# Kernel optimization log

Hardware: AMD Instinct MI355X
Metric: run time of the kernel (lower is better)

## Reference

```python
import jax, jax.numpy as jnp
import numpy as np

B, T, N, A_DIM = 64, 512, 256, 8
TAU, DT, J1 = 10.0, 1.0, 0.1
BUMP_WIDTH_FACTOR = 10.0


def setup_inputs() -> dict:
    key = jax.random.key(0)
    k1, k2, k3 = jax.random.split(key, 3)
    action_signal = jax.random.normal(k1, (B, T, A_DIM), dtype=jnp.float32)
    # learned params, init as in torch: randn / sqrt(N)
    Wo = jax.random.normal(k2, (N, N), dtype=jnp.float32) / np.sqrt(N).astype(np.float32)
    Wa = jax.random.normal(k3, (A_DIM, N, N), dtype=jnp.float32) / np.sqrt(N).astype(np.float32)
    # buffers
    idx = jnp.arange(N, dtype=jnp.float32)
    angle_diff = 2.0 * jnp.pi * (idx[:, None] - idx[None, :]) / N
    W_delta7 = jnp.cos(angle_diff)                       # [N, N]
    J0 = -0.1 * jnp.ones((N, N), dtype=jnp.float32)      # baseline connectivity
    # initial bump at angle pi (create_initial_bump with default r_init=None)
    centers = (jnp.full((B,), jnp.pi, dtype=jnp.float32) * N / (2.0 * jnp.pi))[:, None]
    d = jnp.abs(idx[None, :] - centers)
    dist = jnp.minimum(d, N - d)
    width = N / BUMP_WIDTH_FACTOR
    bump = jnp.exp(-(dist ** 2) / (2.0 * width ** 2))
    r_init = bump / jnp.linalg.norm(bump, axis=1, keepdims=True)  # [B, N]
    return {"action_signal": action_signal, "r_init": r_init, "Wo": Wo,
            "Wa": Wa, "J0": J0, "W_delta7": W_delta7}


def reference(action_signal, r_init, Wo, Wa, J0, W_delta7):
    # W_eff[b] = J0 + J1*Wo + sum_a A[b,t,a] * Wa[a]; never materialize [B,T,N,N]
    W_base = J0 + J1 * Wo                         # [N, N], action-independent part
    leak = jnp.float32(DT / TAU)

    def step(r, A_t):                             # r: [B,N], A_t: [B,A]
        Wr = jnp.einsum('aij,bj->abi', Wa, r)     # [A, B, N] per-action matvec
        rec = r @ W_base.T + jnp.einsum('ba,abi->bi', A_t, Wr)  # [B, N]
        r_new = r + leak * (-r + jnp.tanh(rec))   # leaky-rate update
        d7 = r_new @ W_delta7.T                   # output projection [B, N]
        bump = d7 / jnp.linalg.norm(d7, axis=1, keepdims=True)  # normalized r_delta7
        return r_new, (r_new, bump)

    _, (r_hist, bump_hist) = jax.lax.scan(step, r_init,
                                          jnp.swapaxes(action_signal, 0, 1))
    # scan stacks over time -> [T, B, N]; return [B, T, N]
    return jnp.swapaxes(r_hist, 0, 1), jnp.swapaxes(bump_hist, 0, 1)
```

## Files before the change

### kernel.cpp

```cpp
#include <hip/hip_runtime.h>
#include <math.h>


#define BATCH 64
#define TT    512
#define NN    256
#define ADIM  8
#define NMAT  9
#define ROWS  (NMAT * NN)
#define GROUPS (ROWS / 64)
#define NTHR  576
#define KC    32

__global__ __launch_bounds__(256)
void build_wt_kernel(const float* __restrict__ Wo,
                     const float* __restrict__ Wa,
                     const float* __restrict__ J0,
                     uint4* __restrict__ Wt)
{
  const int q    = blockIdx.x * 256 + threadIdx.x;
  const int lane = q & 63;
  const int kc   = (q >> 6) & 31;
  const int g    = q >> 11;
  const int row  = g * 64 + lane;
  const int mat  = row >> 8;
  const int i    = row & 255;
  const int c0   = kc * 8;
  float v[8];
  if (mat == 0) {
    #pragma unroll
    for (int j = 0; j < 8; ++j)
      v[j] = J0[i * NN + c0 + j] + 0.1f * Wo[i * NN + c0 + j];
  } else {
    const float* src = Wa + ((size_t)(mat - 1) * NN + i) * NN + c0;
    #pragma unroll
    for (int j = 0; j < 8; ++j) v[j] = src[j];
  }
  uint p[4];
  #pragma unroll
  for (int j = 0; j < 4; ++j) {
    _Float16 hl = (_Float16)v[2 * j];
    _Float16 hh = (_Float16)v[2 * j + 1];
    unsigned short sl, sh;
    __builtin_memcpy(&sl, &hl, 2);
    __builtin_memcpy(&sh, &hh, 2);
    p[j] = (uint)sl | ((uint)sh << 16);
  }
  Wt[(size_t)(g * KC + kc) * 64 + lane] = make_uint4(p[0], p[1], p[2], p[3]);
}

__device__ __forceinline__ float f16lo(uint u) {
  unsigned short s = (unsigned short)(u & 0xFFFFu);
  _Float16 h; __builtin_memcpy(&h, &s, 2);
  return (float)h;
}
__device__ __forceinline__ float f16hi(uint u) {
  unsigned short s = (unsigned short)(u >> 16);
  _Float16 h; __builtin_memcpy(&h, &s, 2);
  return (float)h;
}

__device__ __forceinline__ float dot8(uint4 w, float4 ra, float4 rb) {
  float s;
  s  = f16lo(w.x) * ra.x;
  s += f16hi(w.x) * ra.y;
  s += f16lo(w.y) * ra.z;
  s += f16hi(w.y) * ra.w;
  s += f16lo(w.z) * rb.x;
  s += f16hi(w.z) * rb.y;
  s += f16lo(w.w) * rb.z;
  s += f16hi(w.w) * rb.w;
  return s;
}

__global__ __launch_bounds__(NTHR, 1)
void ring_main_kernel(const float* __restrict__ act,
                      const float* __restrict__ r_init,
                      const float* __restrict__ Wd7,
                      const uint4* __restrict__ Wt,
                      float* __restrict__ out)
{
  __shared__ float r_s[NN];
  __shared__ float m_s[ROWS];
  __shared__ float cvec[NN], svec[NN];
  __shared__ float at_s[ADIM];
  __shared__ float cs_s[4][2];
  __shared__ float sums_s[3];

  const int tid  = threadIdx.x;
  const int wv   = tid >> 6;
  const int lane = tid & 63;
  const int b    = blockIdx.x;

  float* out_r = out;
  float* out_b = out + (size_t)BATCH * TT * NN;

  for (int idx = tid; idx < NN; idx += NTHR) {
    cvec[idx] = Wd7[idx * NN];
    svec[idx] = Wd7[idx * NN + 64];
    r_s[idx]  = r_init[b * NN + idx];
  }
  __syncthreads();
  if (tid == 0) {
    float a = 0.f, c2 = 0.f, c = 0.f;
    for (int j = 0; j < NN; ++j) {
      const float cj = cvec[j], sj = svec[j];
      a += cj * cj; c2 += cj * sj; c += sj * sj;
    }
    sums_s[0] = a; sums_s[1] = c2; sums_s[2] = c;
  }
  __syncthreads();

  const int g0 = wv * 4;
  const uint4* base0 = Wt + (size_t)(g0 + 0) * KC * 64 + lane;
  const uint4* base1 = Wt + (size_t)(g0 + 1) * KC * 64 + lane;
  const uint4* base2 = Wt + (size_t)(g0 + 2) * KC * 64 + lane;
  const uint4* base3 = Wt + (size_t)(g0 + 3) * KC * 64 + lane;

  for (int t = 0; t < TT; ++t) {
    if (tid < ADIM) at_s[tid] = act[((size_t)b * TT + t) * ADIM + tid];

    float a0 = 0.f, a1 = 0.f, a2 = 0.f, a3 = 0.f;
    uint4 w0 = base0[0], w1 = base1[0], w2 = base2[0], w3 = base3[0];
    #pragma unroll 4
    for (int k = 0; k < KC; ++k) {
      const float4 ra = *(const float4*)&r_s[k * 8];
      const float4 rb = *(const float4*)&r_s[k * 8 + 4];
      const int kn = (k + 1) & (KC - 1);
      uint4 n0 = base0[kn * 64], n1 = base1[kn * 64];
      uint4 n2 = base2[kn * 64], n3 = base3[kn * 64];
      a0 += dot8(w0, ra, rb);
      a1 += dot8(w1, ra, rb);
      a2 += dot8(w2, ra, rb);
      a3 += dot8(w3, ra, rb);
      w0 = n0; w1 = n1; w2 = n2; w3 = n3;
    }
    m_s[(g0 + 0) * 64 + lane] = a0;
    m_s[(g0 + 1) * 64 + lane] = a1;
    m_s[(g0 + 2) * 64 + lane] = a2;
    m_s[(g0 + 3) * 64 + lane] = a3;
    __syncthreads();

    if (tid < NN) {
      const int i = tid;
      float rec = m_s[i];
      #pragma unroll
      for (int a = 0; a < ADIM; ++a) rec += at_s[a] * m_s[(1 + a) * NN + i];
      const float ro = r_s[i];
      const float rn = ro + 0.1f * (tanhf(rec) - ro);
      r_s[i] = rn;
      out_r[((size_t)b * TT + t) * NN + i] = rn;
      float cp = cvec[i] * rn, sp = svec[i] * rn;
      #pragma unroll
      for (int m = 1; m < 64; m <<= 1) {
        cp += __shfl_xor(cp, m);
        sp += __shfl_xor(sp, m);
      }
      if (lane == 0) { cs_s[wv][0] = cp; cs_s[wv][1] = sp; }
    }
    __syncthreads();

    if (tid < NN) {
      const int i = tid;
      const float C = cs_s[0][0] + cs_s[1][0] + cs_s[2][0] + cs_s[3][0];
      const float S = cs_s[0][1] + cs_s[1][1] + cs_s[2][1] + cs_s[3][1];
      const float n2 = sums_s[0] * C * C + 2.f * sums_s[1] * C * S
                     + sums_s[2] * S * S;
      out_b[((size_t)b * TT + t) * NN + i] =
          (cvec[i] * C + svec[i] * S) * (1.0f / sqrtf(n2));
    }
  }
}

extern "C" void kernel_launch(void* const* d_in, const int* in_sizes, int n_in,
                              void* d_out, int out_size, void* d_ws, size_t ws_size,
                              hipStream_t stream) {
  const float* act    = (const float*)d_in[0];
  const float* r_init = (const float*)d_in[1];
  const float* Wo     = (const float*)d_in[2];
  const float* Wa     = (const float*)d_in[3];
  const float* J0     = (const float*)d_in[4];
  const float* Wd7    = (const float*)d_in[5];
  float* out = (float*)d_out;
  uint4* Wt  = (uint4*)d_ws;

  hipLaunchKernelGGL(build_wt_kernel, dim3(288), dim3(256), 0, stream,
                     Wo, Wa, J0, Wt);
  hipLaunchKernelGGL(ring_main_kernel, dim3(BATCH), dim3(NTHR), 0, stream,
                     act, r_init, Wd7, (const uint4*)Wt, out);
}
```

Baseline: 6.234 ms.

## Keep per-thread weight slices in registers and use fdot2 with split-f16 state

```diff
diff --git a/kernel.cpp b/kernel.cpp
--- a/kernel.cpp
+++ b/kernel.cpp
@@ -8,9 +8,27 @@
 #define ADIM  8
 #define NMAT  9
 #define ROWS  (NMAT * NN)
-#define GROUPS (ROWS / 64)
-#define NTHR  576
-#define KC    32
+#define NTHR  768
+#define KQ    32
+#define REG_KQ2 16
+
+typedef _Float16 half2_t __attribute__((ext_vector_type(2)));
+
+static __device__ __forceinline__ half2_t u2h(unsigned int u) {
+  union { unsigned int u; half2_t h; } c; c.u = u; return c.h;
+}
+
+static __device__ __forceinline__ void dot4(uint4 w, uint4 rh, uint4 rl,
+                                            float& ah, float& al) {
+  ah = __builtin_amdgcn_fdot2(u2h(w.x), u2h(rh.x), ah, false);
+  ah = __builtin_amdgcn_fdot2(u2h(w.y), u2h(rh.y), ah, false);
+  ah = __builtin_amdgcn_fdot2(u2h(w.z), u2h(rh.z), ah, false);
+  ah = __builtin_amdgcn_fdot2(u2h(w.w), u2h(rh.w), ah, false);
+  al = __builtin_amdgcn_fdot2(u2h(w.x), u2h(rl.x), al, false);
+  al = __builtin_amdgcn_fdot2(u2h(w.y), u2h(rl.y), al, false);
+  al = __builtin_amdgcn_fdot2(u2h(w.z), u2h(rl.z), al, false);
+  al = __builtin_amdgcn_fdot2(u2h(w.w), u2h(rl.w), al, false);
+}
 
 __global__ __launch_bounds__(256)
 void build_wt_kernel(const float* __restrict__ Wo,
@@ -18,14 +36,15 @@
                      const float* __restrict__ J0,
                      uint4* __restrict__ Wt)
 {
-  const int q    = blockIdx.x * 256 + threadIdx.x;
-  const int lane = q & 63;
-  const int kc   = (q >> 6) & 31;
-  const int g    = q >> 11;
-  const int row  = g * 64 + lane;
-  const int mat  = row >> 8;
-  const int i    = row & 255;
-  const int c0   = kc * 8;
+  const int q     = blockIdx.x * 256 + threadIdx.x;
+  const int gkq   = q / NTHR;
+  const int tid_t = q - gkq * NTHR;
+  const int g     = gkq >> 5;
+  const int kq    = gkq & 31;
+  const int row   = g * NTHR + tid_t;
+  const int mat   = row >> 8;
+  const int i     = row & 255;
+  const int c0    = kq * 8;
   float v[8];
   if (mat == 0) {
     #pragma unroll
@@ -36,7 +55,7 @@
     #pragma unroll
     for (int j = 0; j < 8; ++j) v[j] = src[j];
   }
-  uint p[4];
+  unsigned int p[4];
   #pragma unroll
   for (int j = 0; j < 4; ++j) {
     _Float16 hl = (_Float16)v[2 * j];
@@ -44,33 +63,9 @@
     unsigned short sl, sh;
     __builtin_memcpy(&sl, &hl, 2);
     __builtin_memcpy(&sh, &hh, 2);
-    p[j] = (uint)sl | ((uint)sh << 16);
-  }
-  Wt[(size_t)(g * KC + kc) * 64 + lane] = make_uint4(p[0], p[1], p[2], p[3]);
-}
-
-__device__ __forceinline__ float f16lo(uint u) {
-  unsigned short s = (unsigned short)(u & 0xFFFFu);
-  _Float16 h; __builtin_memcpy(&h, &s, 2);
-  return (float)h;
-}
-__device__ __forceinline__ float f16hi(uint u) {
-  unsigned short s = (unsigned short)(u >> 16);
-  _Float16 h; __builtin_memcpy(&h, &s, 2);
-  return (float)h;
-}
-
-__device__ __forceinline__ float dot8(uint4 w, float4 ra, float4 rb) {
-  float s;
-  s  = f16lo(w.x) * ra.x;
-  s += f16hi(w.x) * ra.y;
-  s += f16lo(w.y) * ra.z;
-  s += f16hi(w.y) * ra.w;
-  s += f16lo(w.z) * rb.x;
-  s += f16hi(w.z) * rb.y;
-  s += f16lo(w.w) * rb.z;
-  s += f16hi(w.w) * rb.w;
-  return s;
+    p[j] = (unsigned int)sl | ((unsigned int)sh << 16);
+  }
+  Wt[(size_t)gkq * NTHR + tid_t] = make_uint4(p[0], p[1], p[2], p[3]);
 }
 
 __global__ __launch_bounds__(NTHR, 1)
@@ -80,7 +75,8 @@
                       const uint4* __restrict__ Wt,
                       float* __restrict__ out)
 {
-  __shared__ float r_s[NN];
+  __shared__ uint4 rhq[KQ];
+  __shared__ uint4 rlq[KQ];
   __shared__ float m_s[ROWS];
   __shared__ float cvec[NN], svec[NN];
   __shared__ float at_s[ADIM];
@@ -98,7 +94,13 @@
   for (int idx = tid; idx < NN; idx += NTHR) {
     cvec[idx] = Wd7[idx * NN];
     svec[idx] = Wd7[idx * NN + 64];
-    r_s[idx]  = r_init[b * NN + idx];
+  }
+  if (tid < NN) {
+    const float rv = r_init[b * NN + tid];
+    _Float16 h = (_Float16)rv;
+    _Float16 l = (_Float16)((rv - (float)h) * 2048.0f);
+    ((_Float16*)rhq)[tid] = h;
+    ((_Float16*)rlq)[tid] = l;
   }
   __syncthreads();
   if (tid == 0) {
@@ -109,36 +111,44 @@
     }
     sums_s[0] = a; sums_s[1] = c2; sums_s[2] = c;
   }
+
+  uint4 w0[KQ], w1[KQ], w2[REG_KQ2];
+  {
+    const uint4* p0 = Wt + (size_t)0 * KQ * NTHR + tid;
+    const uint4* p1 = Wt + (size_t)1 * KQ * NTHR + tid;
+    const uint4* p2 = Wt + (size_t)2 * KQ * NTHR + tid;
+    #pragma unroll
+    for (int k = 0; k < KQ; ++k) w0[k] = p0[k * NTHR];
+    #pragma unroll
+    for (int k = 0; k < KQ; ++k) w1[k] = p1[k * NTHR];
+    #pragma unroll
+    for (int k = 0; k < REG_KQ2; ++k) w2[k] = p2[k * NTHR];
+  }
+  const uint4* wtail = Wt + ((size_t)2 * KQ + REG_KQ2) * NTHR + tid;
   __syncthreads();
 
-  const int g0 = wv * 4;
-  const uint4* base0 = Wt + (size_t)(g0 + 0) * KC * 64 + lane;
-  const uint4* base1 = Wt + (size_t)(g0 + 1) * KC * 64 + lane;
-  const uint4* base2 = Wt + (size_t)(g0 + 2) * KC * 64 + lane;
-  const uint4* base3 = Wt + (size_t)(g0 + 3) * KC * 64 + lane;
+  const float LSCALE = 1.0f / 2048.0f;
 
   for (int t = 0; t < TT; ++t) {
     if (tid < ADIM) at_s[tid] = act[((size_t)b * TT + t) * ADIM + tid];
 
-    float a0 = 0.f, a1 = 0.f, a2 = 0.f, a3 = 0.f;
-    uint4 w0 = base0[0], w1 = base1[0], w2 = base2[0], w3 = base3[0];
-    #pragma unroll 4
-    for (int k = 0; k < KC; ++k) {
-      const float4 ra = *(const float4*)&r_s[k * 8];
-      const float4 rb = *(const float4*)&r_s[k * 8 + 4];
-      const int kn = (k + 1) & (KC - 1);
-      uint4 n0 = base0[kn * 64], n1 = base1[kn * 64];
-      uint4 n2 = base2[kn * 64], n3 = base3[kn * 64];
-      a0 += dot8(w0, ra, rb);
-      a1 += dot8(w1, ra, rb);
-      a2 += dot8(w2, ra, rb);
-      a3 += dot8(w3, ra, rb);
-      w0 = n0; w1 = n1; w2 = n2; w3 = n3;
-    }
-    m_s[(g0 + 0) * 64 + lane] = a0;
-    m_s[(g0 + 1) * 64 + lane] = a1;
-    m_s[(g0 + 2) * 64 + lane] = a2;
-    m_s[(g0 + 3) * 64 + lane] = a3;
+    uint4 tail[KQ - REG_KQ2];
+    #pragma unroll
+    for (int q = 0; q < KQ - REG_KQ2; ++q) tail[q] = wtail[q * NTHR];
+
+    float ah0 = 0.f, al0 = 0.f, ah1 = 0.f, al1 = 0.f, ah2 = 0.f, al2 = 0.f;
+    #pragma unroll
+    for (int kq = 0; kq < KQ; ++kq) {
+      const uint4 rh = rhq[kq];
+      const uint4 rl = rlq[kq];
+      dot4(w0[kq], rh, rl, ah0, al0);
+      dot4(w1[kq], rh, rl, ah1, al1);
+      if (kq < REG_KQ2) dot4(w2[kq], rh, rl, ah2, al2);
+      else              dot4(tail[kq - REG_KQ2], rh, rl, ah2, al2);
+    }
+    m_s[tid]            = ah0 + al0 * LSCALE;
+    m_s[tid + NTHR]     = ah1 + al1 * LSCALE;
+    m_s[tid + 2 * NTHR] = ah2 + al2 * LSCALE;
     __syncthreads();
 
     if (tid < NN) {
@@ -146,9 +156,9 @@
       float rec = m_s[i];
       #pragma unroll
       for (int a = 0; a < ADIM; ++a) rec += at_s[a] * m_s[(1 + a) * NN + i];
-      const float ro = r_s[i];
+      const float ro = (float)((_Float16*)rhq)[i]
+                     + (float)((_Float16*)rlq)[i] * LSCALE;
       const float rn = ro + 0.1f * (tanhf(rec) - ro);
-      r_s[i] = rn;
       out_r[((size_t)b * TT + t) * NN + i] = rn;
       float cp = cvec[i] * rn, sp = svec[i] * rn;
       #pragma unroll
@@ -156,7 +166,14 @@
         cp += __shfl_xor(cp, m);
         sp += __shfl_xor(sp, m);
       }
+      __syncthreads();
+      _Float16 h = (_Float16)rn;
+      _Float16 l = (_Float16)((rn - (float)h) * 2048.0f);
+      ((_Float16*)rhq)[i] = h;
+      ((_Float16*)rlq)[i] = l;
       if (lane == 0) { cs_s[wv][0] = cp; cs_s[wv][1] = sp; }
+    } else {
+      __syncthreads();
     }
     __syncthreads();
 
```

Result: slower. 12.03 ms (+93.0%).
